# Optimization experiments

Measured on AMD Instinct MI355X. Metric: run time of the kernel, lower is better.

Reference implementation:

```python
import jax, jax.numpy as jnp
import numpy as np

N_NODES = 50000
N_EDGES = 800000
C = 256
R = 4

def setup_inputs() -> dict:
    key = jax.random.key(0)
    ks = jax.random.split(key, 8)
    node_features = jax.random.normal(ks[0], (N_NODES, C), dtype=jnp.float32)
    edge_index = jax.random.randint(ks[1], (2, N_EDGES), 0, N_NODES, dtype=jnp.int64)
    edge_type = jax.random.randint(ks[2], (N_EDGES,), 0, R, dtype=jnp.int64)
    # RGCNConv params (glorot-ish scale)
    s = 1.0 / np.sqrt(C)
    rel_weight = jax.random.normal(ks[3], (R, C, C), dtype=jnp.float32) * s
    root_weight = jax.random.normal(ks[4], (C, C), dtype=jnp.float32) * s
    rgcn_bias = jax.random.normal(ks[5], (C,), dtype=jnp.float32) * 0.01
    att_weight = jax.random.normal(ks[6], (1, 2 * C), dtype=jnp.float32) * (1.0 / np.sqrt(2 * C))
    att_bias = jax.random.normal(ks[7], (1,), dtype=jnp.float32) * 0.01
    return {
        'node_features': node_features,
        'edge_index': edge_index,
        'edge_type': edge_type,
        'rel_weight': rel_weight,
        'root_weight': root_weight,
        'rgcn_bias': rgcn_bias,
        'att_weight': att_weight,
        'att_bias': att_bias,
    }


def _rgcn(node_features, edge_index, edge_type, rel_weight, root_weight, rgcn_bias):
    # PyG RGCNConv: per-relation mean aggregation of x_src @ W_r, plus root transform + bias.
    N = node_features.shape[0]
    src, dst = edge_index[0], edge_index[1]
    out = node_features @ root_weight + rgcn_bias  # [N, O]
    num_rel = rel_weight.shape[0]
    for r in range(num_rel):  # small fixed relation count
        trans = node_features @ rel_weight[r]          # [N, O] node-level transform
        mask = (edge_type == r)
        msg = jnp.where(mask[:, None], trans[src], 0.0)  # [E, O] masked gather
        ssum = jax.ops.segment_sum(msg, dst, num_segments=N)
        cnt = jax.ops.segment_sum(mask.astype(node_features.dtype), dst, num_segments=N)
        out = out + ssum / jnp.maximum(cnt, 1.0)[:, None]  # mean aggr; 0 where no edges
    return out


def reference(node_features, edge_index, edge_type, rel_weight, root_weight, rgcn_bias, att_weight, att_bias):
    u0 = _rgcn(node_features, edge_index, edge_type, rel_weight, root_weight, rgcn_bias)
    cat = jnp.concatenate([u0, node_features], axis=1)  # [N, 2O]
    a = jax.nn.sigmoid(cat @ att_weight.T + att_bias)   # [N, 1]
    h = jnp.tanh(u0) * a + node_features * (1.0 - a)
    return h
```

## Files before the change

kernel.cpp:

```cpp
#include <hip/hip_runtime.h>
#include <hip/hip_bf16.h>

#define C 256
#define BM 64
#define BN 128
#define BK 32
#define NSTEP 40

typedef __attribute__((ext_vector_type(8))) short bf16x8;
typedef __attribute__((ext_vector_type(4))) float f32x4;
typedef __attribute__((ext_vector_type(4))) unsigned short us4;

#define GLL16(g, l)                                                         \
  __builtin_amdgcn_global_load_lds(                                         \
      (const __attribute__((address_space(1))) void*)(g),                   \
      (__attribute__((address_space(3))) void*)(l), 16, 0, 0)

__device__ __forceinline__ float bf2f(unsigned short u) {
  return __uint_as_float(((unsigned int)u) << 16);
}
__device__ __forceinline__ unsigned short f2bf(float f) {
  unsigned int x = __float_as_uint(f);
  unsigned int lsb = (x >> 16) & 1u;
  x += 0x7fffu + lsb;
  return (unsigned short)(x >> 16);
}

__global__ void k_prep_w(const float* __restrict__ rel, const float* __restrict__ root,
                         unsigned short* __restrict__ WT) {
  int b = blockIdx.x;
  int m = b >> 8;
  int c = b & 255;
  int k = threadIdx.x;
  const float* W = (m == 0) ? root : (rel + (size_t)(m - 1) * C * C);
  WT[(size_t)m * C * C + (size_t)c * C + k] = f2bf(W[(size_t)k * C + c]);
}

__global__ void k_cvt_x(const float* __restrict__ X, unsigned short* __restrict__ Xbf,
                        int n_elem, int total) {
  int i = (blockIdx.x * blockDim.x + threadIdx.x) * 4;
  if (i >= total) return;
  us4 o;
  if (i < n_elem) {
    const float4 v = *reinterpret_cast<const float4*>(X + i);
    o.x = f2bf(v.x); o.y = f2bf(v.y); o.z = f2bf(v.z); o.w = f2bf(v.w);
  } else {
    o.x = 0; o.y = 0; o.z = 0; o.w = 0;
  }
  *reinterpret_cast<us4*>(Xbf + i) = o;
}

__global__ void k_hist(const int* __restrict__ edst, int* __restrict__ cnt, int E) {
  int e = blockIdx.x * blockDim.x + threadIdx.x;
  if (e < E) atomicAdd(cnt + edst[e], 1);
}

__global__ void k_scan1(const int* __restrict__ cnt, int* __restrict__ rp,
                        int* __restrict__ bsum, int n) {
  __shared__ int s[512];
  int t = threadIdx.x;
  int i = blockIdx.x * 512 + t;
  int v = (i < n) ? cnt[i] : 0;
  s[t] = v;
  __syncthreads();
  for (int off = 1; off < 512; off <<= 1) {
    int add = (t >= off) ? s[t - off] : 0;
    __syncthreads();
    s[t] += add;
    __syncthreads();
  }
  if (i < n) rp[i] = s[t] - v;
  if (t == 511) bsum[blockIdx.x] = s[511];
}

__global__ void k_scan2(const int* __restrict__ bsum, int* __restrict__ boff,
                        int* __restrict__ rp, int nb, int n) {
  if (threadIdx.x == 0) {
    int run = 0;
    for (int b = 0; b < nb; ++b) { boff[b] = run; run += bsum[b]; }
    rp[n] = run;
  }
}

__global__ void k_scan3(int* __restrict__ rp, const int* __restrict__ boff, int n) {
  int i = blockIdx.x * 512 + threadIdx.x;
  if (i < n) rp[i] += boff[blockIdx.x];
}

__global__ void k_fill(const int* __restrict__ esrc, const int* __restrict__ edst,
                       const int* __restrict__ etype, int* __restrict__ cursor,
                       unsigned int* __restrict__ sorted, int E) {
  int e = blockIdx.x * blockDim.x + threadIdx.x;
  if (e >= E) return;
  int d = edst[e];
  int pos = atomicAdd(cursor + d, 1);
  sorted[pos] = (unsigned int)esrc[e] | ((unsigned int)etype[e] << 28);
}

#define ACC(u, v)                                                            \
  do {                                                                       \
    float f0 = bf2f((v).x), f1 = bf2f((v).y), f2 = bf2f((v).z), f3 = bf2f((v).w); \
    switch ((u) >> 28) {                                                     \
      case 0: a0.x += f0; a0.y += f1; a0.z += f2; a0.w += f3; ++c0; break;   \
      case 1: a1.x += f0; a1.y += f1; a1.z += f2; a1.w += f3; ++c1; break;   \
      case 2: a2.x += f0; a2.y += f1; a2.z += f2; a2.w += f3; ++c2; break;   \
      default: a3.x += f0; a3.y += f1; a3.z += f2; a3.w += f3; ++c3; break;  \
    }                                                                        \
  } while (0)

__global__ void k_gather(const unsigned short* __restrict__ Xbf,
                         const unsigned int* __restrict__ sorted,
                         const int* __restrict__ rp,
                         unsigned short* __restrict__ agm,
                         int N, int rowsPad) {
  int wave = threadIdx.x >> 6;
  int lane = threadIdx.x & 63;
  int dst = blockIdx.x * 4 + wave;
  if (dst >= rowsPad) return;

  if (dst >= N) {
    us4 z; z.x = 0; z.y = 0; z.z = 0; z.w = 0;
    for (int r = 0; r < 4; ++r)
      *reinterpret_cast<us4*>(agm + ((size_t)r * rowsPad + dst) * C + lane * 4) = z;
    return;
  }

  float4 a0 = make_float4(0, 0, 0, 0), a1 = a0, a2 = a0, a3 = a0;
  int c0 = 0, c1 = 0, c2 = 0, c3 = 0;
  int s = rp[dst], e2 = rp[dst + 1];
  const us4* Xv = reinterpret_cast<const us4*>(Xbf);

  int e = s;
  for (; e + 8 <= e2; e += 8) {
    unsigned int u0 = sorted[e],     u1 = sorted[e + 1], u2 = sorted[e + 2], u3 = sorted[e + 3];
    unsigned int u4 = sorted[e + 4], u5 = sorted[e + 5], u6 = sorted[e + 6], u7 = sorted[e + 7];
    us4 v0 = Xv[(size_t)(u0 & 0x0FFFFFFFu) * 64 + lane];
    us4 v1 = Xv[(size_t)(u1 & 0x0FFFFFFFu) * 64 + lane];
    us4 v2 = Xv[(size_t)(u2 & 0x0FFFFFFFu) * 64 + lane];
    us4 v3 = Xv[(size_t)(u3 & 0x0FFFFFFFu) * 64 + lane];
    us4 v4 = Xv[(size_t)(u4 & 0x0FFFFFFFu) * 64 + lane];
    us4 v5 = Xv[(size_t)(u5 & 0x0FFFFFFFu) * 64 + lane];
    us4 v6 = Xv[(size_t)(u6 & 0x0FFFFFFFu) * 64 + lane];
    us4 v7 = Xv[(size_t)(u7 & 0x0FFFFFFFu) * 64 + lane];
    ACC(u0, v0); ACC(u1, v1); ACC(u2, v2); ACC(u3, v3);
    ACC(u4, v4); ACC(u5, v5); ACC(u6, v6); ACC(u7, v7);
  }
  for (; e + 4 <= e2; e += 4) {
    unsigned int u0 = sorted[e], u1 = sorted[e + 1], u2 = sorted[e + 2], u3 = sorted[e + 3];
    us4 v0 = Xv[(size_t)(u0 & 0x0FFFFFFFu) * 64 + lane];
    us4 v1 = Xv[(size_t)(u1 & 0x0FFFFFFFu) * 64 + lane];
    us4 v2 = Xv[(size_t)(u2 & 0x0FFFFFFFu) * 64 + lane];
    us4 v3 = Xv[(size_t)(u3 & 0x0FFFFFFFu) * 64 + lane];
    ACC(u0, v0); ACC(u1, v1); ACC(u2, v2); ACC(u3, v3);
  }
  for (; e < e2; ++e) {
    unsigned int u = sorted[e];
    us4 v = Xv[(size_t)(u & 0x0FFFFFFFu) * 64 + lane];
    ACC(u, v);
  }

  float s0 = 1.0f / (float)max(c0, 1);
  float s1 = 1.0f / (float)max(c1, 1);
  float s2 = 1.0f / (float)max(c2, 1);
  float s3 = 1.0f / (float)max(c3, 1);
  us4 o;
  size_t base = (size_t)dst * C + lane * 4;
  o.x = f2bf(a0.x * s0); o.y = f2bf(a0.y * s0); o.z = f2bf(a0.z * s0); o.w = f2bf(a0.w * s0);
  *reinterpret_cast<us4*>(agm + base) = o;
  o.x = f2bf(a1.x * s1); o.y = f2bf(a1.y * s1); o.z = f2bf(a1.z * s1); o.w = f2bf(a1.w * s1);
  *reinterpret_cast<us4*>(agm + (size_t)rowsPad * C + base) = o;
  o.x = f2bf(a2.x * s2); o.y = f2bf(a2.y * s2); o.z = f2bf(a2.z * s2); o.w = f2bf(a2.w * s2);
  *reinterpret_cast<us4*>(agm + (size_t)2 * rowsPad * C + base) = o;
  o.x = f2bf(a3.x * s3); o.y = f2bf(a3.y * s3); o.z = f2bf(a3.z * s3); o.w = f2bf(a3.w * s3);
  *reinterpret_cast<us4*>(agm + (size_t)3 * rowsPad * C + base) = o;
}

__global__ __launch_bounds__(256) void k_gemm(const unsigned short* __restrict__ Aall,
                                              const unsigned short* __restrict__ WT,
                                              const float* __restrict__ bias,
                                              float* __restrict__ out, int N, int rowsPad) {
  __shared__ unsigned short lds_a[2][BM * BK];
  __shared__ unsigned short lds_b[2][BN * BK];
  int tid = threadIdx.x;
  int wave = tid >> 6, lane = tid & 63;

  int nwg = gridDim.x;
  int orig = blockIdx.x;
  int q = nwg >> 3, r = nwg & 7;
  int xcd = orig & 7, lin = orig >> 3;
  int wgid = (xcd < r ? xcd * (q + 1) : r * (q + 1) + (xcd - r) * q) + lin;

  int mblk = wgid >> 1, nblk = wgid & 1;
  int row0 = mblk * BM, col0 = nblk * BN;
  int wr = wave >> 1, wc = wave & 1;

  int offA = wave * 1024 + lane * 16;
  int arS = offA >> 6;
  int alg8 = ((((offA >> 4) & 3) ^ ((arS >> 1) & 3))) * 8;
  int brS[2], blg8[2];
#pragma unroll
  for (int c2 = 0; c2 < 2; ++c2) {
    int off = (wave * 2 + c2) * 1024 + lane * 16;
    int rr = off >> 6;
    brS[c2] = rr;
    blg8[c2] = ((((off >> 4) & 3) ^ ((rr >> 1) & 3))) * 8;
  }

  int aoff[2], boff[4];
  int kb = (lane >> 4) * 16;
#pragma unroll
  for (int i = 0; i < 2; ++i) {
    int ar = wr * 32 + i * 16 + (lane & 15);
    aoff[i] = ar * 64 + (kb ^ (((ar >> 1) & 3) << 4));
  }
#pragma unroll
  for (int j = 0; j < 4; ++j) {
    int bc = wc * 64 + j * 16 + (lane & 15);
    boff[j] = bc * 64 + (kb ^ (((bc >> 1) & 3) << 4));
  }

  f32x4 acc[2][4];
#pragma unroll
  for (int i = 0; i < 2; ++i)
#pragma unroll
    for (int j = 0; j < 4; ++j) {
      f32x4 z; z[0] = 0.f; z[1] = 0.f; z[2] = 0.f; z[3] = 0.f;
      acc[i][j] = z;
    }

  auto stage = [&](int buf, int ks) {
    int m = ks >> 3;
    int kk = (ks & 7) * BK;
    const unsigned short* Ab = Aall + (size_t)m * rowsPad * C + kk;
    const unsigned short* Bb = WT + (size_t)m * C * C + kk;
    GLL16(Ab + (size_t)(row0 + arS) * C + alg8, (char*)&lds_a[buf][0] + wave * 1024);
#pragma unroll
    for (int c2 = 0; c2 < 2; ++c2)
      GLL16(Bb + (size_t)(col0 + brS[c2]) * C + blg8[c2],
            (char*)&lds_b[buf][0] + (wave * 2 + c2) * 1024);
  };

  stage(0, 0);
  __syncthreads();

#pragma unroll 1
  for (int ks = 0; ks < NSTEP; ++ks) {
    int cur = ks & 1;
    if (ks + 1 < NSTEP) stage(cur ^ 1, ks + 1);
    bf16x8 af[2], bfr[4];
#pragma unroll
    for (int i = 0; i < 2; ++i)
      af[i] = *reinterpret_cast<const bf16x8*>((const char*)&lds_a[cur][0] + aoff[i]);
#pragma unroll
    for (int j = 0; j < 4; ++j)
      bfr[j] = *reinterpret_cast<const bf16x8*>((const char*)&lds_b[cur][0] + boff[j]);
#pragma unroll
    for (int mr = 0; mr < 2; ++mr)
#pragma unroll
      for (int nc = 0; nc < 4; ++nc)
        acc[mr][nc] = __builtin_amdgcn_mfma_f32_16x16x32_bf16(af[mr], bfr[nc], acc[mr][nc], 0, 0, 0);
    __syncthreads();
  }

  int lcol = lane & 15, lrow4 = (lane >> 4) * 4;
#pragma unroll
  for (int mr = 0; mr < 2; ++mr) {
#pragma unroll
    for (int reg = 0; reg < 4; ++reg) {
      int rowg = row0 + wr * 32 + mr * 16 + lrow4 + reg;
      if (rowg < N) {
#pragma unroll
        for (int nc = 0; nc < 4; ++nc) {
          int colg = col0 + wc * 64 + nc * 16 + lcol;
          out[(size_t)rowg * C + colg] = acc[mr][nc][reg] + bias[colg];
        }
      }
    }
  }
}

__global__ void k_gate(const float* __restrict__ X, const float* __restrict__ aw,
                       const float* __restrict__ ab, float* __restrict__ out, int N) {
  int wave = threadIdx.x >> 6, lane = threadIdx.x & 63;
  int node = blockIdx.x * 4 + wave;
  if (node >= N) return;
  const float4* u4 = reinterpret_cast<const float4*>(out + (size_t)node * C);
  const float4* x4 = reinterpret_cast<const float4*>(X + (size_t)node * C);
  float4 u = u4[lane], x = x4[lane];
  const float4* w = reinterpret_cast<const float4*>(aw);
  float4 w1 = w[lane], w2 = w[64 + lane];
  float p = u.x * w1.x + u.y * w1.y + u.z * w1.z + u.w * w1.w
          + x.x * w2.x + x.y * w2.y + x.z * w2.z + x.w * w2.w;
#pragma unroll
  for (int off = 32; off >= 1; off >>= 1) p += __shfl_xor(p, off);
  float a = 1.0f / (1.0f + expf(-(p + ab[0])));
  float b = 1.0f - a;
  float4 h;
  h.x = tanhf(u.x) * a + x.x * b;
  h.y = tanhf(u.y) * a + x.y * b;
  h.z = tanhf(u.z) * a + x.z * b;
  h.w = tanhf(u.w) * a + x.w * b;
  reinterpret_cast<float4*>(out + (size_t)node * C)[lane] = h;
}

extern "C" void kernel_launch(void* const* d_in, const int* in_sizes, int n_in,
                              void* d_out, int out_size, void* d_ws, size_t ws_size,
                              hipStream_t stream) {
  const float* X     = (const float*)d_in[0];
  const int*   eidx  = (const int*)d_in[1];
  const int*   etype = (const int*)d_in[2];
  const float* rel   = (const float*)d_in[3];
  const float* root  = (const float*)d_in[4];
  const float* bias  = (const float*)d_in[5];
  const float* aw    = (const float*)d_in[6];
  const float* ab    = (const float*)d_in[7];
  float* out = (float*)d_out;

  int N = in_sizes[0] / C;
  int E = in_sizes[2];
  int rowsPad = ((N + 127) / 128) * 128;
  const int* esrc = eidx;
  const int* edst = eidx + E;

  char* w = (char*)d_ws;
  size_t off = 0;
  auto alloc = [&](size_t bytes) -> void* {
    void* p = w + off;
    off += (bytes + 255) & ~(size_t)255;
    return p;
  };
  unsigned short* Aall = (unsigned short*)alloc((size_t)5 * rowsPad * C * 2);
  unsigned short* Xbf  = Aall;
  unsigned short* agm  = Aall + (size_t)rowsPad * C;
  unsigned short* WT   = (unsigned short*)alloc((size_t)5 * C * C * 2);
  int* cnt    = (int*)alloc((size_t)N * 4);
  int* rp     = (int*)alloc((size_t)(N + 1) * 4);
  int* cursor = (int*)alloc((size_t)N * 4);
  int* bsum   = (int*)alloc(1024);
  int* boffb  = (int*)alloc(1024);
  unsigned int* sorted = (unsigned int*)alloc((size_t)E * 4);

  hipMemsetAsync(cnt, 0, (size_t)N * 4, stream);
  k_prep_w<<<5 * C, C, 0, stream>>>(rel, root, WT);
  k_cvt_x<<<(rowsPad * C / 4 + 255) / 256, 256, 0, stream>>>(X, Xbf, N * C, rowsPad * C);
  k_hist<<<(E + 255) / 256, 256, 0, stream>>>(edst, cnt, E);
  int NB = (N + 511) / 512;
  k_scan1<<<NB, 512, 0, stream>>>(cnt, rp, bsum, N);
  k_scan2<<<1, 64, 0, stream>>>(bsum, boffb, rp, NB, N);
  k_scan3<<<NB, 512, 0, stream>>>(rp, boffb, N);
  hipMemcpyAsync(cursor, rp, (size_t)N * 4, hipMemcpyDeviceToDevice, stream);
  k_fill<<<(E + 255) / 256, 256, 0, stream>>>(esrc, edst, etype, cursor, sorted, E);
  k_gather<<<rowsPad / 4, 256, 0, stream>>>(Xbf, sorted, rp, agm, N, rowsPad);
  k_gemm<<<(rowsPad / BM) * 2, 256, 0, stream>>>(Aall, WT, bias, out, N, rowsPad);
  k_gate<<<(N + 3) / 4, 256, 0, stream>>>(X, aw, ab, out, N);
}
```

Measured before the change: 271.2 us.

## Fuse gating epilogue into GEMM with full-width tiles and precompute x-attention dot

Widens the GEMM tile to cover all 256 output columns so each block owns whole rows. That lets the attention dot product, sigmoid gate, tanh and blend run in the GEMM epilogue, and the separate gate kernel along with its round trip of the intermediate output through memory is removed. The x-half of the attention dot is computed during the bf16 conversion kernel. The cursor copy is folded into the scan kernel, which drops a memcpy. The trade-off is more accumulators per thread and larger LDS, which may lower occupancy, and the grid has half as many blocks.

```diff
diff --git a/kernel.cpp b/kernel.cpp
--- a/kernel.cpp
+++ b/kernel.cpp
@@ -3,7 +3,7 @@
 
 #define C 256
 #define BM 64
-#define BN 128
+#define BN 256
 #define BK 32
 #define NSTEP 40
 
@@ -36,18 +36,27 @@
   WT[(size_t)m * C * C + (size_t)c * C + k] = f2bf(W[(size_t)k * C + c]);
 }
 
-__global__ void k_cvt_x(const float* __restrict__ X, unsigned short* __restrict__ Xbf,
-                        int n_elem, int total) {
-  int i = (blockIdx.x * blockDim.x + threadIdx.x) * 4;
-  if (i >= total) return;
+__global__ void k_cvt_x(const float* __restrict__ X, const float* __restrict__ attw,
+                        unsigned short* __restrict__ Xbf, float* __restrict__ ax2,
+                        int N, int rowsPad) {
+  int wave = threadIdx.x >> 6, lane = threadIdx.x & 63;
+  int row = blockIdx.x * 4 + wave;
+  if (row >= rowsPad) return;
+  if (row >= N) {
+    us4 z; z.x = 0; z.y = 0; z.z = 0; z.w = 0;
+    reinterpret_cast<us4*>(Xbf + (size_t)row * C)[lane] = z;
+    if (lane == 0) ax2[row] = 0.f;
+    return;
+  }
+  float4 v = reinterpret_cast<const float4*>(X + (size_t)row * C)[lane];
+  float4 w2 = reinterpret_cast<const float4*>(attw + C)[lane];
   us4 o;
-  if (i < n_elem) {
-    const float4 v = *reinterpret_cast<const float4*>(X + i);
-    o.x = f2bf(v.x); o.y = f2bf(v.y); o.z = f2bf(v.z); o.w = f2bf(v.w);
-  } else {
-    o.x = 0; o.y = 0; o.z = 0; o.w = 0;
-  }
-  *reinterpret_cast<us4*>(Xbf + i) = o;
+  o.x = f2bf(v.x); o.y = f2bf(v.y); o.z = f2bf(v.z); o.w = f2bf(v.w);
+  reinterpret_cast<us4*>(Xbf + (size_t)row * C)[lane] = o;
+  float p = v.x * w2.x + v.y * w2.y + v.z * w2.z + v.w * w2.w;
+#pragma unroll
+  for (int m = 32; m >= 1; m >>= 1) p += __shfl_xor(p, m);
+  if (lane == 0) ax2[row] = p;
 }
 
 __global__ void k_hist(const int* __restrict__ edst, int* __restrict__ cnt, int E) {
@@ -82,9 +91,14 @@
   }
 }
 
-__global__ void k_scan3(int* __restrict__ rp, const int* __restrict__ boff, int n) {
+__global__ void k_scan3(int* __restrict__ rp, const int* __restrict__ boff,
+                        int* __restrict__ cursor, int n) {
   int i = blockIdx.x * 512 + threadIdx.x;
-  if (i < n) rp[i] += boff[blockIdx.x];
+  if (i < n) {
+    int v = rp[i] + boff[blockIdx.x];
+    rp[i] = v;
+    cursor[i] = v;
+  }
 }
 
 __global__ void k_fill(const int* __restrict__ esrc, const int* __restrict__ edst,
@@ -175,53 +189,42 @@
   *reinterpret_cast<us4*>(agm + (size_t)3 * rowsPad * C + base) = o;
 }
 
-__global__ __launch_bounds__(256) void k_gemm(const unsigned short* __restrict__ Aall,
-                                              const unsigned short* __restrict__ WT,
-                                              const float* __restrict__ bias,
-                                              float* __restrict__ out, int N, int rowsPad) {
+__global__ __launch_bounds__(256, 4) void k_gemm(
+    const unsigned short* __restrict__ Aall, const unsigned short* __restrict__ WT,
+    const float* __restrict__ bias, const float* __restrict__ X,
+    const float* __restrict__ ax2, const float* __restrict__ attw,
+    const float* __restrict__ abp, float* __restrict__ out, int N, int rowsPad) {
   __shared__ unsigned short lds_a[2][BM * BK];
   __shared__ unsigned short lds_b[2][BN * BK];
   int tid = threadIdx.x;
   int wave = tid >> 6, lane = tid & 63;
-
-  int nwg = gridDim.x;
-  int orig = blockIdx.x;
-  int q = nwg >> 3, r = nwg & 7;
-  int xcd = orig & 7, lin = orig >> 3;
-  int wgid = (xcd < r ? xcd * (q + 1) : r * (q + 1) + (xcd - r) * q) + lin;
-
-  int mblk = wgid >> 1, nblk = wgid & 1;
-  int row0 = mblk * BM, col0 = nblk * BN;
-  int wr = wave >> 1, wc = wave & 1;
-
-  int offA = wave * 1024 + lane * 16;
-  int arS = offA >> 6;
-  int alg8 = ((((offA >> 4) & 3) ^ ((arS >> 1) & 3))) * 8;
-  int brS[2], blg8[2];
-#pragma unroll
-  for (int c2 = 0; c2 < 2; ++c2) {
-    int off = (wave * 2 + c2) * 1024 + lane * 16;
-    int rr = off >> 6;
-    brS[c2] = rr;
-    blg8[c2] = ((((off >> 4) & 3) ^ ((rr >> 1) & 3))) * 8;
-  }
-
-  int aoff[2], boff[4];
+  int row0 = blockIdx.x * BM;
+  int wc = wave;
+  int lcol = lane & 15;
+
+  int arS = wave * 16 + (lane >> 2);
+  int alg8 = (((lane & 3) ^ ((arS >> 1) & 3))) * 8;
+  int bcS[4], blg8[4];
+#pragma unroll
+  for (int c4 = 0; c4 < 4; ++c4) {
+    int cc = (wave * 4 + c4) * 16 + (lane >> 2);
+    bcS[c4] = cc;
+    blg8[c4] = (((lane & 3) ^ ((cc >> 1) & 3))) * 8;
+  }
+
+  int aoff[4], boff[4];
   int kb = (lane >> 4) * 16;
 #pragma unroll
-  for (int i = 0; i < 2; ++i) {
-    int ar = wr * 32 + i * 16 + (lane & 15);
+  for (int i = 0; i < 4; ++i) {
+    int ar = i * 16 + lcol;
     aoff[i] = ar * 64 + (kb ^ (((ar >> 1) & 3) << 4));
-  }
-#pragma unroll
-  for (int j = 0; j < 4; ++j) {
-    int bc = wc * 64 + j * 16 + (lane & 15);
-    boff[j] = bc * 64 + (kb ^ (((bc >> 1) & 3) << 4));
-  }
-
-  f32x4 acc[2][4];
-#pragma unroll
-  for (int i = 0; i < 2; ++i)
+    int bc = wc * 64 + i * 16 + lcol;
+    boff[i] = bc * 64 + (kb ^ (((bc >> 1) & 3) << 4));
+  }
+
+  f32x4 acc[4][4];
+#pragma unroll
+  for (int i = 0; i < 4; ++i)
 #pragma unroll
     for (int j = 0; j < 4; ++j) {
       f32x4 z; z[0] = 0.f; z[1] = 0.f; z[2] = 0.f; z[3] = 0.f;
@@ -235,9 +238,9 @@
     const unsigned short* Bb = WT + (size_t)m * C * C + kk;
     GLL16(Ab + (size_t)(row0 + arS) * C + alg8, (char*)&lds_a[buf][0] + wave * 1024);
 #pragma unroll
-    for (int c2 = 0; c2 < 2; ++c2)
-      GLL16(Bb + (size_t)(col0 + brS[c2]) * C + blg8[c2],
-            (char*)&lds_b[buf][0] + (wave * 2 + c2) * 1024);
+    for (int c4 = 0; c4 < 4; ++c4)
+      GLL16(Bb + (size_t)bcS[c4] * C + blg8[c4],
+            (char*)&lds_b[buf][0] + (wave * 4 + c4) * 1024);
   };
 
   stage(0, 0);
@@ -247,60 +250,78 @@
   for (int ks = 0; ks < NSTEP; ++ks) {
     int cur = ks & 1;
     if (ks + 1 < NSTEP) stage(cur ^ 1, ks + 1);
-    bf16x8 af[2], bfr[4];
-#pragma unroll
-    for (int i = 0; i < 2; ++i)
-      af[i] = *reinterpret_cast<const bf16x8*>((const char*)&lds_a[cur][0] + aoff[i]);
-#pragma unroll
-    for (int j = 0; j < 4; ++j)
-      bfr[j] = *reinterpret_cast<const bf16x8*>((const char*)&lds_b[cur][0] + boff[j]);
-#pragma unroll
-    for (int mr = 0; mr < 2; ++mr)
+    bf16x8 af[4], bfr[4];
+#pragma unroll
+    for (int i = 0; i < 4; ++i) {
+      af[i]  = *reinterpret_cast<const bf16x8*>((const char*)&lds_a[cur][0] + aoff[i]);
+      bfr[i] = *reinterpret_cast<const bf16x8*>((const char*)&lds_b[cur][0] + boff[i]);
+    }
+#pragma unroll
+    for (int mr = 0; mr < 4; ++mr)
 #pragma unroll
       for (int nc = 0; nc < 4; ++nc)
         acc[mr][nc] = __builtin_amdgcn_mfma_f32_16x16x32_bf16(af[mr], bfr[nc], acc[mr][nc], 0, 0, 0);
     __syncthreads();
   }
 
-  int lcol = lane & 15, lrow4 = (lane >> 4) * 4;
-#pragma unroll
-  for (int mr = 0; mr < 2; ++mr) {
+  float awv[4], biasv[4];
+#pragma unroll
+  for (int nc = 0; nc < 4; ++nc) {
+    int colg = wc * 64 + nc * 16 + lcol;
+    awv[nc] = attw[colg];
+    biasv[nc] = bias[colg];
+  }
+#pragma unroll
+  for (int mr = 0; mr < 4; ++mr)
+#pragma unroll
+    for (int nc = 0; nc < 4; ++nc)
+#pragma unroll
+      for (int reg = 0; reg < 4; ++reg)
+        acc[mr][nc][reg] += biasv[nc];
+
+  float prow[4][4];
+#pragma unroll
+  for (int mr = 0; mr < 4; ++mr)
 #pragma unroll
     for (int reg = 0; reg < 4; ++reg) {
-      int rowg = row0 + wr * 32 + mr * 16 + lrow4 + reg;
-      if (rowg < N) {
-#pragma unroll
-        for (int nc = 0; nc < 4; ++nc) {
-          int colg = col0 + wc * 64 + nc * 16 + lcol;
-          out[(size_t)rowg * C + colg] = acc[mr][nc][reg] + bias[colg];
-        }
+      float p = acc[mr][0][reg] * awv[0] + acc[mr][1][reg] * awv[1]
+              + acc[mr][2][reg] * awv[2] + acc[mr][3][reg] * awv[3];
+      p += __shfl_xor(p, 1); p += __shfl_xor(p, 2);
+      p += __shfl_xor(p, 4); p += __shfl_xor(p, 8);
+      prow[mr][reg] = p;
+    }
+
+  float* rsum = reinterpret_cast<float*>(&lds_a[0][0]);
+  if (lcol == 0) {
+    int q = lane >> 4;
+#pragma unroll
+    for (int mr = 0; mr < 4; ++mr)
+#pragma unroll
+      for (int reg = 0; reg < 4; ++reg)
+        rsum[(mr * 16 + q * 4 + reg) * 4 + wave] = prow[mr][reg];
+  }
+  __syncthreads();
+
+  float ab0 = abp[0];
+#pragma unroll
+  for (int mr = 0; mr < 4; ++mr) {
+#pragma unroll
+    for (int reg = 0; reg < 4; ++reg) {
+      int row = mr * 16 + (lane >> 4) * 4 + reg;
+      int rowg = row0 + row;
+      if (rowg >= N) continue;
+      float4 rs = *reinterpret_cast<float4*>(&rsum[row * 4]);
+      float t = rs.x + rs.y + rs.z + rs.w + ax2[rowg] + ab0;
+      float a = 1.0f / (1.0f + expf(-t));
+      float b = 1.0f - a;
+#pragma unroll
+      for (int nc = 0; nc < 4; ++nc) {
+        int colg = wc * 64 + nc * 16 + lcol;
+        float x = X[(size_t)rowg * C + colg];
+        out[(size_t)rowg * C + colg] = tanhf(acc[mr][nc][reg]) * a + x * b;
       }
     }
   }
-}
-
-__global__ void k_gate(const float* __restrict__ X, const float* __restrict__ aw,
-                       const float* __restrict__ ab, float* __restrict__ out, int N) {
-  int wave = threadIdx.x >> 6, lane = threadIdx.x & 63;
-  int node = blockIdx.x * 4 + wave;
-  if (node >= N) return;
-  const float4* u4 = reinterpret_cast<const float4*>(out + (size_t)node * C);
-  const float4* x4 = reinterpret_cast<const float4*>(X + (size_t)node * C);
-  float4 u = u4[lane], x = x4[lane];
-  const float4* w = reinterpret_cast<const float4*>(aw);
-  float4 w1 = w[lane], w2 = w[64 + lane];
-  float p = u.x * w1.x + u.y * w1.y + u.z * w1.z + u.w * w1.w
-          + x.x * w2.x + x.y * w2.y + x.z * w2.z + x.w * w2.w;
-#pragma unroll
-  for (int off = 32; off >= 1; off >>= 1) p += __shfl_xor(p, off);
-  float a = 1.0f / (1.0f + expf(-(p + ab[0])));
-  float b = 1.0f - a;
-  float4 h;
-  h.x = tanhf(u.x) * a + x.x * b;
-  h.y = tanhf(u.y) * a + x.y * b;
-  h.z = tanhf(u.z) * a + x.z * b;
-  h.w = tanhf(u.w) * a + x.w * b;
-  reinterpret_cast<float4*>(out + (size_t)node * C)[lane] = h;
 }
 
 extern "C" void kernel_launch(void* const* d_in, const int* in_sizes, int n_in,
@@ -312,13 +333,13 @@
   const float* rel   = (const float*)d_in[3];
   const float* root  = (const float*)d_in[4];
   const float* bias  = (const float*)d_in[5];
-  const float* aw    = (const float*)d_in[6];
+  const float* attw  = (const float*)d_in[6];
   const float* ab    = (const float*)d_in[7];
   float* out = (float*)d_out;
 
   int N = in_sizes[0] / C;
   int E = in_sizes[2];
-  int rowsPad = ((N + 127) / 128) * 128;
+  int rowsPad = ((N + 63) / 64) * 64;
   const int* esrc = eidx;
   const int* edst = eidx + E;
 
@@ -333,6 +354,7 @@
   unsigned short* Xbf  = Aall;
   unsigned short* agm  = Aall + (size_t)rowsPad * C;
   unsigned short* WT   = (unsigned short*)alloc((size_t)5 * C * C * 2);
+  float* ax2  = (float*)alloc((size_t)rowsPad * 4);
   int* cnt    = (int*)alloc((size_t)N * 4);
   int* rp     = (int*)alloc((size_t)(N + 1) * 4);
   int* cursor = (int*)alloc((size_t)N * 4);
@@ -342,15 +364,13 @@
 
   hipMemsetAsync(cnt, 0, (size_t)N * 4, stream);
   k_prep_w<<<5 * C, C, 0, stream>>>(rel, root, WT);
-  k_cvt_x<<<(rowsPad * C / 4 + 255) / 256, 256, 0, stream>>>(X, Xbf, N * C, rowsPad * C);
+  k_cvt_x<<<rowsPad / 4, 256, 0, stream>>>(X, attw, Xbf, ax2, N, rowsPad);
   k_hist<<<(E + 255) / 256, 256, 0, stream>>>(edst, cnt, E);
   int NB = (N + 511) / 512;
   k_scan1<<<NB, 512, 0, stream>>>(cnt, rp, bsum, N);
   k_scan2<<<1, 64, 0, stream>>>(bsum, boffb, rp, NB, N);
-  k_scan3<<<NB, 512, 0, stream>>>(rp, boffb, N);
-  hipMemcpyAsync(cursor, rp, (size_t)N * 4, hipMemcpyDeviceToDevice, stream);
+  k_scan3<<<NB, 512, 0, stream>>>(rp, boffb, cursor, N);
   k_fill<<<(E + 255) / 256, 256, 0, stream>>>(esrc, edst, etype, cursor, sorted, E);
   k_gather<<<rowsPad / 4, 256, 0, stream>>>(Xbf, sorted, rp, agm, N, rowsPad);
-  k_gemm<<<(rowsPad / BM) * 2, 256, 0, stream>>>(Aall, WT, bias, out, N, rowsPad);
-  k_gate<<<(N + 3) / 4, 256, 0, stream>>>(X, aw, ab, out, N);
-}
+  k_gemm<<<rowsPad / BM, 256, 0, stream>>>(Aall, WT, bias, X, ax2, attw, ab, out, N, rowsPad);
+}
```

Result: slower. 279.7 us (+3.1%).

## Load GEMM B fragments directly into registers and fuse cursor copy into scan

Applied to the files above, without the earlier changes.

The GEMM no longer stages weight tiles through LDS. Each lane loads its bf16x8 B fragment straight from global memory into registers, one step ahead of use, which cuts LDS traffic and footprint and may raise occupancy. The cost is uncoalesced-ish global loads of the small, cache-resident weight matrix. Separately, the scan's final pass now writes the cursor array directly, which removes a device-to-device memcpy.

```diff
diff --git a/kernel.cpp b/kernel.cpp
--- a/kernel.cpp
+++ b/kernel.cpp
@@ -82,9 +82,14 @@
   }
 }
 
-__global__ void k_scan3(int* __restrict__ rp, const int* __restrict__ boff, int n) {
+__global__ void k_scan3(int* __restrict__ rp, const int* __restrict__ boff,
+                        int* __restrict__ cursor, int n) {
   int i = blockIdx.x * 512 + threadIdx.x;
-  if (i < n) rp[i] += boff[blockIdx.x];
+  if (i < n) {
+    int v = rp[i] + boff[blockIdx.x];
+    rp[i] = v;
+    cursor[i] = v;
+  }
 }
 
 __global__ void k_fill(const int* __restrict__ esrc, const int* __restrict__ edst,
@@ -175,49 +180,36 @@
   *reinterpret_cast<us4*>(agm + (size_t)3 * rowsPad * C + base) = o;
 }
 
-__global__ __launch_bounds__(256) void k_gemm(const unsigned short* __restrict__ Aall,
-                                              const unsigned short* __restrict__ WT,
-                                              const float* __restrict__ bias,
-                                              float* __restrict__ out, int N, int rowsPad) {
+__global__ __launch_bounds__(256) void k_gemm(
+    const unsigned short* __restrict__ Aall, const unsigned short* __restrict__ WT,
+    const float* __restrict__ bias, float* __restrict__ out, int N, int rowsPad) {
   __shared__ unsigned short lds_a[2][BM * BK];
-  __shared__ unsigned short lds_b[2][BN * BK];
   int tid = threadIdx.x;
   int wave = tid >> 6, lane = tid & 63;
 
-  int nwg = gridDim.x;
-  int orig = blockIdx.x;
+  int nwg = gridDim.x, orig = blockIdx.x;
   int q = nwg >> 3, r = nwg & 7;
   int xcd = orig & 7, lin = orig >> 3;
   int wgid = (xcd < r ? xcd * (q + 1) : r * (q + 1) + (xcd - r) * q) + lin;
-
   int mblk = wgid >> 1, nblk = wgid & 1;
   int row0 = mblk * BM, col0 = nblk * BN;
-  int wr = wave >> 1, wc = wave & 1;
+  int wr = wave >> 1, wc = wave & 1, lcol = lane & 15;
 
   int offA = wave * 1024 + lane * 16;
   int arS = offA >> 6;
   int alg8 = ((((offA >> 4) & 3) ^ ((arS >> 1) & 3))) * 8;
-  int brS[2], blg8[2];
-#pragma unroll
-  for (int c2 = 0; c2 < 2; ++c2) {
-    int off = (wave * 2 + c2) * 1024 + lane * 16;
-    int rr = off >> 6;
-    brS[c2] = rr;
-    blg8[c2] = ((((off >> 4) & 3) ^ ((rr >> 1) & 3))) * 8;
-  }
-
-  int aoff[2], boff[4];
+
+  int aoff[2];
   int kb = (lane >> 4) * 16;
 #pragma unroll
   for (int i = 0; i < 2; ++i) {
-    int ar = wr * 32 + i * 16 + (lane & 15);
+    int ar = wr * 32 + i * 16 + lcol;
     aoff[i] = ar * 64 + (kb ^ (((ar >> 1) & 3) << 4));
   }
-#pragma unroll
-  for (int j = 0; j < 4; ++j) {
-    int bc = wc * 64 + j * 16 + (lane & 15);
-    boff[j] = bc * 64 + (kb ^ (((bc >> 1) & 3) << 4));
-  }
+  int bcol[4];
+#pragma unroll
+  for (int j = 0; j < 4; ++j) bcol[j] = col0 + wc * 64 + j * 16 + lcol;
+  int kq = (lane >> 4) * 8;
 
   f32x4 acc[2][4];
 #pragma unroll
@@ -228,41 +220,42 @@
       acc[i][j] = z;
     }
 
-  auto stage = [&](int buf, int ks) {
-    int m = ks >> 3;
-    int kk = (ks & 7) * BK;
+  auto stageA = [&](int buf, int ks) {
+    int m = ks >> 3, kk = (ks & 7) * BK;
     const unsigned short* Ab = Aall + (size_t)m * rowsPad * C + kk;
-    const unsigned short* Bb = WT + (size_t)m * C * C + kk;
     GLL16(Ab + (size_t)(row0 + arS) * C + alg8, (char*)&lds_a[buf][0] + wave * 1024);
-#pragma unroll
-    for (int c2 = 0; c2 < 2; ++c2)
-      GLL16(Bb + (size_t)(col0 + brS[c2]) * C + blg8[c2],
-            (char*)&lds_b[buf][0] + (wave * 2 + c2) * 1024);
   };
-
-  stage(0, 0);
+  auto loadB = [&](int ks, int j) {
+    int m = ks >> 3, kk = (ks & 7) * BK;
+    return *reinterpret_cast<const bf16x8*>(
+        WT + (size_t)m * 65536 + (size_t)bcol[j] * 256 + kk + kq);
+  };
+
+  stageA(0, 0);
+  bf16x8 b0 = loadB(0, 0), b1 = loadB(0, 1), b2 = loadB(0, 2), b3 = loadB(0, 3);
   __syncthreads();
 
 #pragma unroll 1
   for (int ks = 0; ks < NSTEP; ++ks) {
     int cur = ks & 1;
-    if (ks + 1 < NSTEP) stage(cur ^ 1, ks + 1);
-    bf16x8 af[2], bfr[4];
-#pragma unroll
-    for (int i = 0; i < 2; ++i)
-      af[i] = *reinterpret_cast<const bf16x8*>((const char*)&lds_a[cur][0] + aoff[i]);
-#pragma unroll
-    for (int j = 0; j < 4; ++j)
-      bfr[j] = *reinterpret_cast<const bf16x8*>((const char*)&lds_b[cur][0] + boff[j]);
-#pragma unroll
-    for (int mr = 0; mr < 2; ++mr)
-#pragma unroll
-      for (int nc = 0; nc < 4; ++nc)
-        acc[mr][nc] = __builtin_amdgcn_mfma_f32_16x16x32_bf16(af[mr], bfr[nc], acc[mr][nc], 0, 0, 0);
+    int ks1 = (ks + 1 < NSTEP) ? ks + 1 : NSTEP - 1;
+    if (ks + 1 < NSTEP) stageA(cur ^ 1, ks + 1);
+    bf16x8 n0 = loadB(ks1, 0), n1 = loadB(ks1, 1), n2 = loadB(ks1, 2), n3 = loadB(ks1, 3);
+    bf16x8 af0 = *reinterpret_cast<const bf16x8*>((const char*)&lds_a[cur][0] + aoff[0]);
+    bf16x8 af1 = *reinterpret_cast<const bf16x8*>((const char*)&lds_a[cur][0] + aoff[1]);
+    acc[0][0] = __builtin_amdgcn_mfma_f32_16x16x32_bf16(af0, b0, acc[0][0], 0, 0, 0);
+    acc[0][1] = __builtin_amdgcn_mfma_f32_16x16x32_bf16(af0, b1, acc[0][1], 0, 0, 0);
+    acc[0][2] = __builtin_amdgcn_mfma_f32_16x16x32_bf16(af0, b2, acc[0][2], 0, 0, 0);
+    acc[0][3] = __builtin_amdgcn_mfma_f32_16x16x32_bf16(af0, b3, acc[0][3], 0, 0, 0);
+    acc[1][0] = __builtin_amdgcn_mfma_f32_16x16x32_bf16(af1, b0, acc[1][0], 0, 0, 0);
+    acc[1][1] = __builtin_amdgcn_mfma_f32_16x16x32_bf16(af1, b1, acc[1][1], 0, 0, 0);
+    acc[1][2] = __builtin_amdgcn_mfma_f32_16x16x32_bf16(af1, b2, acc[1][2], 0, 0, 0);
+    acc[1][3] = __builtin_amdgcn_mfma_f32_16x16x32_bf16(af1, b3, acc[1][3], 0, 0, 0);
     __syncthreads();
-  }
-
-  int lcol = lane & 15, lrow4 = (lane >> 4) * 4;
+    b0 = n0; b1 = n1; b2 = n2; b3 = n3;
+  }
+
+  int lrow4 = (lane >> 4) * 4;
 #pragma unroll
   for (int mr = 0; mr < 2; ++mr) {
 #pragma unroll
@@ -312,7 +305,7 @@
   const float* rel   = (const float*)d_in[3];
   const float* root  = (const float*)d_in[4];
   const float* bias  = (const float*)d_in[5];
-  const float* aw    = (const float*)d_in[6];
+  const float* attw  = (const float*)d_in[6];
   const float* ab    = (const float*)d_in[7];
   float* out = (float*)d_out;
 
@@ -347,10 +340,9 @@
   int NB = (N + 511) / 512;
   k_scan1<<<NB, 512, 0, stream>>>(cnt, rp, bsum, N);
   k_scan2<<<1, 64, 0, stream>>>(bsum, boffb, rp, NB, N);
-  k_scan3<<<NB, 512, 0, stream>>>(rp, boffb, N);
-  hipMemcpyAsync(cursor, rp, (size_t)N * 4, hipMemcpyDeviceToDevice, stream);
+  k_scan3<<<NB, 512, 0, stream>>>(rp, boffb, cursor, N);
   k_fill<<<(E + 255) / 256, 256, 0, stream>>>(esrc, edst, etype, cursor, sorted, E);
   k_gather<<<rowsPad / 4, 256, 0, stream>>>(Xbf, sorted, rp, agm, N, rowsPad);
   k_gemm<<<(rowsPad / BM) * 2, 256, 0, stream>>>(Aall, WT, bias, out, N, rowsPad);
-  k_gate<<<(N + 3) / 4, 256, 0, stream>>>(X, aw, ab, out, N);
-}
+  k_gate<<<(N + 3) / 4, 256, 0, stream>>>(X, attw, ab, out, N);
+}
```

Measured after the change: 350.1 us. 1.29x slower.

## Interleave activations into one K=1280 row layout and fuse prep kernels

Applied to the files above, without the earlier changes.

Stores the bf16 copy of X and the four per-relation mean aggregates side by side in a single row-major matrix with K=1280, and the weights as a matching [256,1280] transposed matrix, so the GEMM walks one contiguous K range per row. It merges weight conversion, X conversion and count zeroing into a single launch, and writes the cursor copy inside the scan kernel in place of a separate memcpy. This removes launch and memset/memcpy overhead and simplifies GEMM addressing. The cost is that the gather now reads X rows at a 2560-byte stride instead of a 512-byte one.

```diff
diff --git a/kernel.cpp b/kernel.cpp
--- a/kernel.cpp
+++ b/kernel.cpp
@@ -2,6 +2,7 @@
 #include <hip/hip_bf16.h>
 
 #define C 256
+#define KTOT 1280
 #define BM 64
 #define BN 128
 #define BK 32
@@ -26,28 +27,28 @@
   return (unsigned short)(x >> 16);
 }
 
-__global__ void k_prep_w(const float* __restrict__ rel, const float* __restrict__ root,
-                         unsigned short* __restrict__ WT) {
-  int b = blockIdx.x;
-  int m = b >> 8;
-  int c = b & 255;
-  int k = threadIdx.x;
-  const float* W = (m == 0) ? root : (rel + (size_t)(m - 1) * C * C);
-  WT[(size_t)m * C * C + (size_t)c * C + k] = f2bf(W[(size_t)k * C + c]);
-}
-
-__global__ void k_cvt_x(const float* __restrict__ X, unsigned short* __restrict__ Xbf,
-                        int n_elem, int total) {
-  int i = (blockIdx.x * blockDim.x + threadIdx.x) * 4;
-  if (i >= total) return;
-  us4 o;
-  if (i < n_elem) {
-    const float4 v = *reinterpret_cast<const float4*>(X + i);
-    o.x = f2bf(v.x); o.y = f2bf(v.y); o.z = f2bf(v.z); o.w = f2bf(v.w);
+__global__ void k_pre(const float* __restrict__ X, const float* __restrict__ rel,
+                      const float* __restrict__ root, unsigned short* __restrict__ Aall,
+                      unsigned short* __restrict__ WT, int* __restrict__ cnt,
+                      int N, int rowsPad) {
+  int b = blockIdx.x, t = threadIdx.x;
+  if (b < 1280) {
+    int m = b >> 8, c = b & 255;
+    const float* W = (m == 0) ? root : (rel + (size_t)(m - 1) * C * C);
+    WT[(size_t)c * KTOT + m * C + t] = f2bf(W[(size_t)t * C + c]);
+  } else if (b < 1280 + (rowsPad >> 2)) {
+    int row = (b - 1280) * 4 + (t >> 6);
+    int lane = t & 63;
+    us4 o;
+    if (row < N) {
+      float4 v = reinterpret_cast<const float4*>(X + (size_t)row * C)[lane];
+      o.x = f2bf(v.x); o.y = f2bf(v.y); o.z = f2bf(v.z); o.w = f2bf(v.w);
+    } else { o.x = 0; o.y = 0; o.z = 0; o.w = 0; }
+    *reinterpret_cast<us4*>(Aall + (size_t)row * KTOT + lane * 4) = o;
   } else {
-    o.x = 0; o.y = 0; o.z = 0; o.w = 0;
-  }
-  *reinterpret_cast<us4*>(Xbf + i) = o;
+    int i = (b - 1280 - (rowsPad >> 2)) * 256 + t;
+    if (i < N) cnt[i] = 0;
+  }
 }
 
 __global__ void k_hist(const int* __restrict__ edst, int* __restrict__ cnt, int E) {
@@ -82,9 +83,14 @@
   }
 }
 
-__global__ void k_scan3(int* __restrict__ rp, const int* __restrict__ boff, int n) {
+__global__ void k_scan3(int* __restrict__ rp, const int* __restrict__ boff,
+                        int* __restrict__ cursor, int n) {
   int i = blockIdx.x * 512 + threadIdx.x;
-  if (i < n) rp[i] += boff[blockIdx.x];
+  if (i < n) {
+    int v = rp[i] + boff[blockIdx.x];
+    rp[i] = v;
+    cursor[i] = v;
+  }
 }
 
 __global__ void k_fill(const int* __restrict__ esrc, const int* __restrict__ edst,
@@ -108,54 +114,52 @@
     }                                                                        \
   } while (0)
 
-__global__ void k_gather(const unsigned short* __restrict__ Xbf,
+__global__ void k_gather(unsigned short* __restrict__ Aall,
                          const unsigned int* __restrict__ sorted,
-                         const int* __restrict__ rp,
-                         unsigned short* __restrict__ agm,
-                         int N, int rowsPad) {
+                         const int* __restrict__ rp, int N, int rowsPad) {
   int wave = threadIdx.x >> 6;
   int lane = threadIdx.x & 63;
   int dst = blockIdx.x * 4 + wave;
   if (dst >= rowsPad) return;
+  us4* agv = reinterpret_cast<us4*>(Aall);
 
   if (dst >= N) {
     us4 z; z.x = 0; z.y = 0; z.z = 0; z.w = 0;
-    for (int r = 0; r < 4; ++r)
-      *reinterpret_cast<us4*>(agm + ((size_t)r * rowsPad + dst) * C + lane * 4) = z;
+    for (int r = 1; r <= 4; ++r)
+      agv[(size_t)dst * 320 + r * 64 + lane] = z;
     return;
   }
 
   float4 a0 = make_float4(0, 0, 0, 0), a1 = a0, a2 = a0, a3 = a0;
   int c0 = 0, c1 = 0, c2 = 0, c3 = 0;
   int s = rp[dst], e2 = rp[dst + 1];
-  const us4* Xv = reinterpret_cast<const us4*>(Xbf);
 
   int e = s;
   for (; e + 8 <= e2; e += 8) {
     unsigned int u0 = sorted[e],     u1 = sorted[e + 1], u2 = sorted[e + 2], u3 = sorted[e + 3];
     unsigned int u4 = sorted[e + 4], u5 = sorted[e + 5], u6 = sorted[e + 6], u7 = sorted[e + 7];
-    us4 v0 = Xv[(size_t)(u0 & 0x0FFFFFFFu) * 64 + lane];
-    us4 v1 = Xv[(size_t)(u1 & 0x0FFFFFFFu) * 64 + lane];
-    us4 v2 = Xv[(size_t)(u2 & 0x0FFFFFFFu) * 64 + lane];
-    us4 v3 = Xv[(size_t)(u3 & 0x0FFFFFFFu) * 64 + lane];
-    us4 v4 = Xv[(size_t)(u4 & 0x0FFFFFFFu) * 64 + lane];
-    us4 v5 = Xv[(size_t)(u5 & 0x0FFFFFFFu) * 64 + lane];
-    us4 v6 = Xv[(size_t)(u6 & 0x0FFFFFFFu) * 64 + lane];
-    us4 v7 = Xv[(size_t)(u7 & 0x0FFFFFFFu) * 64 + lane];
+    us4 v0 = agv[(size_t)(u0 & 0x0FFFFFFFu) * 320 + lane];
+    us4 v1 = agv[(size_t)(u1 & 0x0FFFFFFFu) * 320 + lane];
+    us4 v2 = agv[(size_t)(u2 & 0x0FFFFFFFu) * 320 + lane];
+    us4 v3 = agv[(size_t)(u3 & 0x0FFFFFFFu) * 320 + lane];
+    us4 v4 = agv[(size_t)(u4 & 0x0FFFFFFFu) * 320 + lane];
+    us4 v5 = agv[(size_t)(u5 & 0x0FFFFFFFu) * 320 + lane];
+    us4 v6 = agv[(size_t)(u6 & 0x0FFFFFFFu) * 320 + lane];
+    us4 v7 = agv[(size_t)(u7 & 0x0FFFFFFFu) * 320 + lane];
     ACC(u0, v0); ACC(u1, v1); ACC(u2, v2); ACC(u3, v3);
     ACC(u4, v4); ACC(u5, v5); ACC(u6, v6); ACC(u7, v7);
   }
   for (; e + 4 <= e2; e += 4) {
     unsigned int u0 = sorted[e], u1 = sorted[e + 1], u2 = sorted[e + 2], u3 = sorted[e + 3];
-    us4 v0 = Xv[(size_t)(u0 & 0x0FFFFFFFu) * 64 + lane];
-    us4 v1 = Xv[(size_t)(u1 & 0x0FFFFFFFu) * 64 + lane];
-    us4 v2 = Xv[(size_t)(u2 & 0x0FFFFFFFu) * 64 + lane];
-    us4 v3 = Xv[(size_t)(u3 & 0x0FFFFFFFu) * 64 + lane];
+    us4 v0 = agv[(size_t)(u0 & 0x0FFFFFFFu) * 320 + lane];
+    us4 v1 = agv[(size_t)(u1 & 0x0FFFFFFFu) * 320 + lane];
+    us4 v2 = agv[(size_t)(u2 & 0x0FFFFFFFu) * 320 + lane];
+    us4 v3 = agv[(size_t)(u3 & 0x0FFFFFFFu) * 320 + lane];
     ACC(u0, v0); ACC(u1, v1); ACC(u2, v2); ACC(u3, v3);
   }
   for (; e < e2; ++e) {
     unsigned int u = sorted[e];
-    us4 v = Xv[(size_t)(u & 0x0FFFFFFFu) * 64 + lane];
+    us4 v = agv[(size_t)(u & 0x0FFFFFFFu) * 320 + lane];
     ACC(u, v);
   }
 
@@ -164,58 +168,56 @@
   float s2 = 1.0f / (float)max(c2, 1);
   float s3 = 1.0f / (float)max(c3, 1);
   us4 o;
-  size_t base = (size_t)dst * C + lane * 4;
+  size_t base = (size_t)dst * 320 + lane;
   o.x = f2bf(a0.x * s0); o.y = f2bf(a0.y * s0); o.z = f2bf(a0.z * s0); o.w = f2bf(a0.w * s0);
-  *reinterpret_cast<us4*>(agm + base) = o;
+  agv[base + 64] = o;
   o.x = f2bf(a1.x * s1); o.y = f2bf(a1.y * s1); o.z = f2bf(a1.z * s1); o.w = f2bf(a1.w * s1);
-  *reinterpret_cast<us4*>(agm + (size_t)rowsPad * C + base) = o;
+  agv[base + 128] = o;
   o.x = f2bf(a2.x * s2); o.y = f2bf(a2.y * s2); o.z = f2bf(a2.z * s2); o.w = f2bf(a2.w * s2);
-  *reinterpret_cast<us4*>(agm + (size_t)2 * rowsPad * C + base) = o;
+  agv[base + 192] = o;
   o.x = f2bf(a3.x * s3); o.y = f2bf(a3.y * s3); o.z = f2bf(a3.z * s3); o.w = f2bf(a3.w * s3);
-  *reinterpret_cast<us4*>(agm + (size_t)3 * rowsPad * C + base) = o;
-}
-
-__global__ __launch_bounds__(256) void k_gemm(const unsigned short* __restrict__ Aall,
-                                              const unsigned short* __restrict__ WT,
-                                              const float* __restrict__ bias,
-                                              float* __restrict__ out, int N, int rowsPad) {
+  agv[base + 256] = o;
+}
+
+__global__ __launch_bounds__(256) void k_gemm(
+    const unsigned short* __restrict__ Aall, const unsigned short* __restrict__ WT,
+    const float* __restrict__ bias, float* __restrict__ out, int N, int rowsPad) {
   __shared__ unsigned short lds_a[2][BM * BK];
   __shared__ unsigned short lds_b[2][BN * BK];
   int tid = threadIdx.x;
   int wave = tid >> 6, lane = tid & 63;
 
-  int nwg = gridDim.x;
-  int orig = blockIdx.x;
+  int nwg = gridDim.x, orig = blockIdx.x;
   int q = nwg >> 3, r = nwg & 7;
   int xcd = orig & 7, lin = orig >> 3;
   int wgid = (xcd < r ? xcd * (q + 1) : r * (q + 1) + (xcd - r) * q) + lin;
-
   int mblk = wgid >> 1, nblk = wgid & 1;
   int row0 = mblk * BM, col0 = nblk * BN;
-  int wr = wave >> 1, wc = wave & 1;
+  int wr = wave >> 1, wc = wave & 1, lcol = lane & 15;
 
   int offA = wave * 1024 + lane * 16;
   int arS = offA >> 6;
   int alg8 = ((((offA >> 4) & 3) ^ ((arS >> 1) & 3))) * 8;
-  int brS[2], blg8[2];
+  const unsigned short* aSrc = Aall + (size_t)(row0 + arS) * KTOT + alg8;
+  const unsigned short* bSrc[2];
 #pragma unroll
   for (int c2 = 0; c2 < 2; ++c2) {
     int off = (wave * 2 + c2) * 1024 + lane * 16;
     int rr = off >> 6;
-    brS[c2] = rr;
-    blg8[c2] = ((((off >> 4) & 3) ^ ((rr >> 1) & 3))) * 8;
+    int lg8 = ((((off >> 4) & 3) ^ ((rr >> 1) & 3))) * 8;
+    bSrc[c2] = WT + (size_t)(col0 + rr) * KTOT + lg8;
   }
 
   int aoff[2], boff[4];
   int kb = (lane >> 4) * 16;
 #pragma unroll
   for (int i = 0; i < 2; ++i) {
-    int ar = wr * 32 + i * 16 + (lane & 15);
+    int ar = wr * 32 + i * 16 + lcol;
     aoff[i] = ar * 64 + (kb ^ (((ar >> 1) & 3) << 4));
   }
 #pragma unroll
   for (int j = 0; j < 4; ++j) {
-    int bc = wc * 64 + j * 16 + (lane & 15);
+    int bc = wc * 64 + j * 16 + lcol;
     boff[j] = bc * 64 + (kb ^ (((bc >> 1) & 3) << 4));
   }
 
@@ -229,15 +231,10 @@
     }
 
   auto stage = [&](int buf, int ks) {
-    int m = ks >> 3;
-    int kk = (ks & 7) * BK;
-    const unsigned short* Ab = Aall + (size_t)m * rowsPad * C + kk;
-    const unsigned short* Bb = WT + (size_t)m * C * C + kk;
-    GLL16(Ab + (size_t)(row0 + arS) * C + alg8, (char*)&lds_a[buf][0] + wave * 1024);
-#pragma unroll
-    for (int c2 = 0; c2 < 2; ++c2)
-      GLL16(Bb + (size_t)(col0 + brS[c2]) * C + blg8[c2],
-            (char*)&lds_b[buf][0] + (wave * 2 + c2) * 1024);
+    int kofs = ks * BK;
+    GLL16(aSrc + kofs, (char*)&lds_a[buf][0] + wave * 1024);
+    GLL16(bSrc[0] + kofs, (char*)&lds_b[buf][0] + (wave * 2) * 1024);
+    GLL16(bSrc[1] + kofs, (char*)&lds_b[buf][0] + (wave * 2 + 1) * 1024);
   };
 
   stage(0, 0);
@@ -262,7 +259,7 @@
     __syncthreads();
   }
 
-  int lcol = lane & 15, lrow4 = (lane >> 4) * 4;
+  int lrow4 = (lane >> 4) * 4;
 #pragma unroll
   for (int mr = 0; mr < 2; ++mr) {
 #pragma unroll
@@ -312,7 +309,7 @@
   const float* rel   = (const float*)d_in[3];
   const float* root  = (const float*)d_in[4];
   const float* bias  = (const float*)d_in[5];
-  const float* aw    = (const float*)d_in[6];
+  const float* attw  = (const float*)d_in[6];
   const float* ab    = (const float*)d_in[7];
   float* out = (float*)d_out;
 
@@ -329,10 +326,8 @@
     off += (bytes + 255) & ~(size_t)255;
     return p;
   };
-  unsigned short* Aall = (unsigned short*)alloc((size_t)5 * rowsPad * C * 2);
-  unsigned short* Xbf  = Aall;
-  unsigned short* agm  = Aall + (size_t)rowsPad * C;
-  unsigned short* WT   = (unsigned short*)alloc((size_t)5 * C * C * 2);
+  unsigned short* Aall = (unsigned short*)alloc((size_t)rowsPad * KTOT * 2);
+  unsigned short* WT   = (unsigned short*)alloc((size_t)C * KTOT * 2);
   int* cnt    = (int*)alloc((size_t)N * 4);
   int* rp     = (int*)alloc((size_t)(N + 1) * 4);
   int* cursor = (int*)alloc((size_t)N * 4);
@@ -340,17 +335,15 @@
   int* boffb  = (int*)alloc(1024);
   unsigned int* sorted = (unsigned int*)alloc((size_t)E * 4);
 
-  hipMemsetAsync(cnt, 0, (size_t)N * 4, stream);
-  k_prep_w<<<5 * C, C, 0, stream>>>(rel, root, WT);
-  k_cvt_x<<<(rowsPad * C / 4 + 255) / 256, 256, 0, stream>>>(X, Xbf, N * C, rowsPad * C);
+  int preBlocks = 1280 + (rowsPad >> 2) + (N + 255) / 256;
+  k_pre<<<preBlocks, 256, 0, stream>>>(X, rel, root, Aall, WT, cnt, N, rowsPad);
   k_hist<<<(E + 255) / 256, 256, 0, stream>>>(edst, cnt, E);
   int NB = (N + 511) / 512;
   k_scan1<<<NB, 512, 0, stream>>>(cnt, rp, bsum, N);
   k_scan2<<<1, 64, 0, stream>>>(bsum, boffb, rp, NB, N);
-  k_scan3<<<NB, 512, 0, stream>>>(rp, boffb, N);
-  hipMemcpyAsync(cursor, rp, (size_t)N * 4, hipMemcpyDeviceToDevice, stream);
+  k_scan3<<<NB, 512, 0, stream>>>(rp, boffb, cursor, N);
   k_fill<<<(E + 255) / 256, 256, 0, stream>>>(esrc, edst, etype, cursor, sorted, E);
-  k_gather<<<rowsPad / 4, 256, 0, stream>>>(Xbf, sorted, rp, agm, N, rowsPad);
+  k_gather<<<rowsPad / 4, 256, 0, stream>>>(Aall, sorted, rp, N, rowsPad);
   k_gemm<<<(rowsPad / BM) * 2, 256, 0, stream>>>(Aall, WT, bias, out, N, rowsPad);
-  k_gate<<<(N + 3) / 4, 256, 0, stream>>>(X, aw, ab, out, N);
-}
+  k_gate<<<(N + 3) / 4, 256, 0, stream>>>(X, attw, ab, out, N);
+}
```

Result: no change. 272.2 us (+0.4%).
